# Kernel tuning notes

Hardware: AMD Instinct MI355X
Metric: run time of the kernel (lower is better)

Reference implementation:

```python
import jax, jax.numpy as jnp
import numpy as np

EPS = 1e-5
THRESHOLD = 0.2987


def conv3x3(x, w, stride=1):
    # x: [N,C,H,W], w: [O,I,3,3]
    return jax.lax.conv_general_dilated(
        x, w, window_strides=(stride, stride), padding=((1, 1), (1, 1)),
        dimension_numbers=("NCHW", "OIHW", "NCHW"))


def batchnorm_train(x, gamma, beta):
    # training-mode BN: batch statistics over (N,H,W), biased variance
    mean = jnp.mean(x, axis=(0, 2, 3), keepdims=True)
    var = jnp.var(x, axis=(0, 2, 3), keepdims=True)
    xhat = (x - mean) * jax.lax.rsqrt(var + EPS)
    return xhat * gamma[None, :, None, None] + beta[None, :, None, None]


def setup_inputs() -> dict:
    key = jax.random.key(0)
    k = jax.random.split(key, 7)
    N, C, H, W = 64, 128, 64, 64
    x = jax.random.normal(k[0], (N, C, H, W), dtype=jnp.float32)
    w1 = jax.random.normal(k[1], (C, C, 3, 3), dtype=jnp.float32) * (1.0 / np.sqrt(C * 9))
    gamma1 = jnp.ones((C,), dtype=jnp.float32)
    beta1 = jnp.zeros((C,), dtype=jnp.float32)
    w2 = jax.random.normal(k[2], (C, C, 3, 3), dtype=jnp.float32) * (1.0 / np.sqrt(C * 9))
    gamma2 = jnp.ones((C,), dtype=jnp.float32)
    beta2 = jnp.zeros((C,), dtype=jnp.float32)
    return {"x": x, "w1": w1, "gamma1": gamma1, "beta1": beta1,
            "w2": w2, "gamma2": gamma2, "beta2": beta2}


def reference(x, w1, gamma1, beta1, w2, gamma2, beta2):
    shortcut = x  # stride=1, no down_sample
    out = conv3x3(x, w1, stride=1)
    out = batchnorm_train(out, gamma1, beta1)
    out = jax.nn.relu(out)
    # per-(batch,channel) mean over H,W; zero channels whose mean < threshold
    channel_means = jnp.mean(out, axis=(2, 3))               # [N, C]
    mask = (channel_means >= THRESHOLD).astype(out.dtype)     # [N, C]
    out = out * mask[:, :, None, None]
    out = conv3x3(out, w2, stride=1)
    out = batchnorm_train(out, gamma2, beta2)
    out = out + shortcut
    out = jax.nn.relu(out)
    return out
```

## Files before the change

### kernel.cpp

```cpp
#include <hip/hip_runtime.h>

typedef short short8 __attribute__((ext_vector_type(8)));
typedef short short4v __attribute__((ext_vector_type(4)));
typedef float f32x4 __attribute__((ext_vector_type(4)));
typedef unsigned int u32;

#define EPSF 1e-5f
#define THRF 0.2987f

constexpr int N_ = 64, C_ = 128;
constexpr int PLANE = 4096;
constexpr size_t TENSOR = (size_t)N_ * C_ * PLANE;
constexpr int NHW = N_ * PLANE;
constexpr int PUNITS = 66 * 66 * 8;

__device__ __forceinline__ unsigned short f2bf(float f) {
    unsigned u = __float_as_uint(f);
    u += 0x7fffu + ((u >> 16) & 1u);
    return (unsigned short)(u >> 16);
}
__device__ __forceinline__ float bf2f(unsigned short h) {
    return __uint_as_float((unsigned)h << 16);
}
__device__ __forceinline__ void gld16(const unsigned short* g, unsigned short* l) {
    __builtin_amdgcn_global_load_lds(
        (const __attribute__((address_space(1))) u32*)g,
        (__attribute__((address_space(3))) u32*)l, 16, 0, 0);
}

__global__ __launch_bounds__(256) void prep_w_k(const float* __restrict__ w1,
                                                const float* __restrict__ w2,
                                                unsigned short* __restrict__ Wt1,
                                                unsigned short* __restrict__ Wt2) {
    int idx = blockIdx.x * 256 + threadIdx.x;
    const int sel = idx >= 147456;
    const float* src = sel ? w2 : w1;
    unsigned short* dst = sel ? Wt2 : Wt1;
    const int r = idx - sel * 147456;
    const int tap = r >> 14;
    const int rem = r & 16383;
    const int co = rem >> 7, ci = rem & 127;
    const int half = ci >> 6, csh = (ci >> 5) & 1;
    const int s = half * 18 + tap * 2 + csh;
    dst[(size_t)s * 4096 + co * 32 + (ci & 31)] = f2bf(src[(co * 128 + ci) * 9 + tap]);
}

__global__ __launch_bounds__(256) void zero_border_k(unsigned short* __restrict__ io) {
    int idx = blockIdx.x * 256 + threadIdx.x;
    if (idx >= 266240) return;
    const int plane = idx / 2080;
    const int t = idx - plane * 2080;
    int sp;
    if (t < 528) sp = t >> 3;
    else if (t < 1056) sp = 65 * 66 + ((t - 528) >> 3);
    else if (t < 1568) sp = (((t - 1056) >> 3) + 1) * 66;
    else sp = (((t - 1568) >> 3) + 1) * 66 + 65;
    const size_t off = ((size_t)plane * PUNITS + sp * 8 + (t & 7)) * 8;
    *(short8*)&io[off] = (short8){0, 0, 0, 0, 0, 0, 0, 0};
}

__global__ __launch_bounds__(256) void to_nhwc_k(const float* __restrict__ src,
                                                 unsigned short* __restrict__ dst) {
    __shared__ __align__(16) unsigned short tl[64 * 40];
    const int b = blockIdx.x;
    const int c0 = (b & 3) * 32;
    const int h  = (b >> 2) & 63;
    const int n  = b >> 8;
    const int t  = threadIdx.x;
    for (int i = t; i < 512; i += 256) {
        const int cl = i >> 4;
        const int c  = c0 + cl;
        const int w4 = (i & 15) * 4;
        float4 v = *(const float4*)&src[(size_t)(n * 128 + c) * 4096 + h * 64 + w4];
        tl[(w4 + 0) * 40 + cl] = f2bf(v.x);
        tl[(w4 + 1) * 40 + cl] = f2bf(v.y);
        tl[(w4 + 2) * 40 + cl] = f2bf(v.z);
        tl[(w4 + 3) * 40 + cl] = f2bf(v.w);
    }
    __syncthreads();
    const int w = t >> 2, cs = t & 3;
    short8 v = *(const short8*)&tl[w * 40 + cs * 8];
    const int c = c0 + cs * 8;
    const int half = c >> 6, cig = (c >> 3) & 7;
    const int colp = w + 1, rowp = h + 1;
    const size_t off = ((size_t)(half * 64 + n) * PUNITS
                        + (size_t)(rowp * 66 + colp) * 8 + (cig ^ (colp & 7))) * 8;
    *(short8*)&dst[off] = v;
}

template <int STAGE>
__global__ __launch_bounds__(256, 3) void conv_mfma_k(
    const unsigned short* __restrict__ inT, const unsigned short* __restrict__ Wt,
    const float* __restrict__ msA, const float* __restrict__ mhA,
    unsigned short* __restrict__ outB, float* __restrict__ part) {
    __shared__ __align__(16) unsigned short sIn[2112 * 8];
    __shared__ float fS[256], fQ[256];

    const int b  = (blockIdx.x & 7) * 256 + (blockIdx.x >> 3);
    const int h0 = (b & 31) * 2;
    const int n  = b >> 5;
    const int tid  = threadIdx.x;
    const int lane = tid & 63;
    const int wid  = tid >> 6;
    const int co_base = (wid >> 1) * 64;
    const int px_base = (wid & 1) * 64;
    const int lr = lane & 15;
    const int lg = lane >> 4;

    f32x4 acc[4][4];
#pragma unroll
    for (int i = 0; i < 4; ++i)
#pragma unroll
        for (int j = 0; j < 4; ++j) acc[i][j] = (f32x4){0.f, 0.f, 0.f, 0.f};

    const int nc = n * 128;
    const unsigned short* wlane = Wt + (size_t)(co_base + lr) * 32 + lg * 8;

    int ldsQ[4][2][3];
#pragma unroll
    for (int j = 0; j < 4; ++j) {
        const int px = px_base + j * 16 + lr;
        const int r = px >> 6, c = px & 63;
#pragma unroll
        for (int csh = 0; csh < 2; ++csh)
#pragma unroll
            for (int dc = 0; dc < 3; ++dc) {
                const int cig = csh * 4 + lg;
                ldsQ[j][csh][dc] = (r * 66 + c + dc) * 128 + (cig ^ ((c + dc) & 7)) * 16;
            }
    }

    auto stage_in = [&](int half) {
        const unsigned short* src =
            inT + ((size_t)(half * 64 + n) * PUNITS + (size_t)h0 * 66 * 8) * 8;
        if (STAGE == 1) {
            for (int c = wid; c < 33; c += 4)
                gld16(src + (c * 64 + lane) * 8, &sIn[c * 512]);
        } else {
            const int ncb = nc + half * 64;
            for (int i = tid; i < 2112; i += 256) {
                const int sp = i >> 3, ul = i & 7;
                const int rq = sp / 66;
                const int colp = sp - rq * 66;
                const int rp = h0 + rq;
                short8 v = {0, 0, 0, 0, 0, 0, 0, 0};
                if (rp != 0 && rp != 65 && colp != 0 && colp != 65) {
                    v = *(const short8*)&src[i * 8];
                    const int cig = ul ^ (colp & 7);
                    const int cb = ncb + cig * 8;
                    const float4 m0 = *(const float4*)&msA[cb];
                    const float4 m1 = *(const float4*)&msA[cb + 4];
                    const float4 a0 = *(const float4*)&mhA[cb];
                    const float4 a1 = *(const float4*)&mhA[cb + 4];
                    short8 w;
                    w[0] = (short)f2bf(fmaxf(fmaf(bf2f((unsigned short)v[0]), m0.x, a0.x), 0.f));
                    w[1] = (short)f2bf(fmaxf(fmaf(bf2f((unsigned short)v[1]), m0.y, a0.y), 0.f));
                    w[2] = (short)f2bf(fmaxf(fmaf(bf2f((unsigned short)v[2]), m0.z, a0.z), 0.f));
                    w[3] = (short)f2bf(fmaxf(fmaf(bf2f((unsigned short)v[3]), m0.w, a0.w), 0.f));
                    w[4] = (short)f2bf(fmaxf(fmaf(bf2f((unsigned short)v[4]), m1.x, a1.x), 0.f));
                    w[5] = (short)f2bf(fmaxf(fmaf(bf2f((unsigned short)v[5]), m1.y, a1.y), 0.f));
                    w[6] = (short)f2bf(fmaxf(fmaf(bf2f((unsigned short)v[6]), m1.z, a1.z), 0.f));
                    w[7] = (short)f2bf(fmaxf(fmaf(bf2f((unsigned short)v[7]), m1.w, a1.w), 0.f));
                    v = w;
                }
                *(short8*)&sIn[i * 8] = v;
            }
        }
    };

    auto ldw2 = [&](short8* dst, const unsigned short* p) {
#pragma unroll
        for (int i = 0; i < 4; ++i)
            dst[i] = *(const short8*)&p[i * 512];
    };
    auto ldb = [&](short8* bfv, int dr, int dc, int csh) {
#pragma unroll
        for (int j = 0; j < 4; ++j)
            bfv[j] = *(const short8*)((const char*)sIn + ldsQ[j][csh][dc] + dr * 8448);
    };
    auto mm = [&](short8* af, short8* bfv) {
        __builtin_amdgcn_s_setprio(1);
#pragma unroll
        for (int i = 0; i < 4; ++i)
#pragma unroll
            for (int j = 0; j < 4; ++j)
                acc[i][j] = __builtin_amdgcn_mfma_f32_16x16x32_bf16(af[i], bfv[j],
                                                                    acc[i][j], 0, 0, 0);
        __builtin_amdgcn_s_setprio(0);
    };

    short8 afA[4], afB[4], bfv[4];
    const unsigned short* wpA = wlane;
    const unsigned short* wpB = wlane + 4096;

    stage_in(0);
    ldw2(afA, wpA);
    ldw2(afB, wpB);
    __syncthreads();

#pragma unroll
    for (int half = 0; half < 2; ++half) {
#pragma unroll
        for (int it = 0; it < 9; ++it) {
            const int dr = it / 3, dc = it - dr * 3;
            ldb(bfv, dr, dc, 0);
            mm(afA, bfv);
            if (it < 8) { wpA += 8192; ldw2(afA, wpA); }
            ldb(bfv, dr, dc, 1);
            mm(afB, bfv);
            if (it < 8) { wpB += 8192; ldw2(afB, wpB); }
        }
        if (half == 0) {
            wpA += 8192; ldw2(afA, wpA);
            wpB += 8192; ldw2(afB, wpB);
            __syncthreads();
            stage_in(1);
            __syncthreads();
        }
    }

#pragma unroll
    for (int i = 0; i < 4; ++i)
#pragma unroll
        for (int q = 0; q < 4; ++q) {
            float v = acc[i][0][q] + acc[i][1][q] + acc[i][2][q] + acc[i][3][q];
            float w = acc[i][0][q] * acc[i][0][q] + acc[i][1][q] * acc[i][1][q]
                    + acc[i][2][q] * acc[i][2][q] + acc[i][3][q] * acc[i][3][q];
#pragma unroll
            for (int m = 1; m < 16; m <<= 1) {
                v += __shfl_xor(v, m);
                w += __shfl_xor(w, m);
            }
            if (lr == 0) {
                const int colocal = i * 16 + lg * 4 + q;
                fS[wid * 64 + colocal] = v;
                fQ[wid * 64 + colocal] = w;
            }
        }
    __syncthreads();
    if (tid < 128) {
        const int grp = tid >> 6, cl = tid & 63;
        part[(size_t)b * 256 + tid]       = fS[(grp * 2) * 64 + cl] + fS[(grp * 2 + 1) * 64 + cl];
        part[(size_t)b * 256 + 128 + tid] = fQ[(grp * 2) * 64 + cl] + fQ[(grp * 2 + 1) * 64 + cl];
    }

    if (STAGE == 1) {
        const int h = h0 + (px_base >> 6);
        const int rowp = h + 1;
        const size_t plane = (size_t)((co_base >> 6) * 64 + n) * PUNITS * 8;
        const int pg = lg >> 1;
#pragma unroll
        for (int j = 0; j < 4; ++j) {
            const int w = j * 16 + lr;
            const int colp = w + 1;
            const size_t spoff = plane + (size_t)(rowp * 66 + colp) * 8 * 8;
#pragma unroll
            for (int i = 0; i < 4; ++i) {
                u32 p0 = ((u32)f2bf(acc[i][j][1]) << 16) | f2bf(acc[i][j][0]);
                u32 p1 = ((u32)f2bf(acc[i][j][3]) << 16) | f2bf(acc[i][j][2]);
                const u32 q0 = __shfl_xor(p0, 16);
                const u32 q1 = __shfl_xor(p1, 16);
                if ((lg & 1) == 0) {
                    const int cig = (i * 2 + pg) & 7;
                    u32 st4[4] = {p0, p1, q0, q1};
                    *(short8*)&outB[spoff + (size_t)(cig ^ (colp & 7)) * 8] =
                        *(const short8*)st4;
                }
            }
        }
    } else {
        const size_t outN = (size_t)n * 128 * 4096;
#pragma unroll
        for (int i = 0; i < 4; ++i) {
            const int cob = co_base + i * 16 + lg * 4;
#pragma unroll
            for (int q = 0; q < 4; ++q) {
                unsigned short* op = outB + outN + (size_t)(cob + q) * 4096
                                     + h0 * 64 + px_base + lr;
#pragma unroll
                for (int j = 0; j < 4; ++j) op[j * 16] = f2bf(acc[i][j][q]);
            }
        }
    }
}

__global__ __launch_bounds__(256) void bn_finalize_k(const float* __restrict__ part,
                                                     const float* __restrict__ gamma,
                                                     const float* __restrict__ beta,
                                                     float* __restrict__ st) {
    const int c = blockIdx.x;
    float s = 0.f, q = 0.f;
    for (int b = threadIdx.x; b < 2048; b += 256) {
        s += part[(size_t)b * 256 + c];
        q += part[(size_t)b * 256 + 128 + c];
    }
    __shared__ float rs[256], rq[256];
    rs[threadIdx.x] = s; rq[threadIdx.x] = q;
    __syncthreads();
    for (int o = 128; o > 0; o >>= 1) {
        if (threadIdx.x < o) {
            rs[threadIdx.x] += rs[threadIdx.x + o];
            rq[threadIdx.x] += rq[threadIdx.x + o];
        }
        __syncthreads();
    }
    if (threadIdx.x == 0) {
        const float inv  = 1.f / (float)NHW;
        const float mean = rs[0] * inv;
        const float var  = rq[0] * inv - mean * mean;
        const float sc   = gamma[c] * rsqrtf(var + EPSF);
        st[c]       = sc;
        st[C_ + c]  = fmaf(-mean, sc, beta[c]);
    }
}

__global__ __launch_bounds__(256) void maskpart_k(const unsigned short* __restrict__ y1,
                                                  const float* __restrict__ st,
                                                  float* __restrict__ qsum) {
    const int blk = blockIdx.x;
    const int n = blk >> 3, half = (blk >> 2) & 1, rq = blk & 3;
    const int t = threadIdx.x;
    const int colg = t & 63;
    const int p = t >> 6;
    const int colp = 1 + colg;
    float scv[2][8], shv[2][8], a[2][8];
#pragma unroll
    for (int k = 0; k < 2; ++k)
#pragma unroll
        for (int e = 0; e < 8; ++e) {
            const int c = half * 64 + (2 * p + k) * 8 + e;
            scv[k][e] = st[c];
            shv[k][e] = st[128 + c];
            a[k][e] = 0.f;
        }
    const size_t plane = (size_t)(half * 64 + n) * PUNITS * 8;
    for (int rowp = rq * 16 + 1; rowp <= rq * 16 + 16; ++rowp) {
        const int sp = rowp * 66 + colp;
#pragma unroll
        for (int k = 0; k < 2; ++k) {
            const int cig = 2 * p + k;
            short8 v = *(const short8*)&y1[plane + ((size_t)sp * 8 + (cig ^ (colp & 7))) * 8];
#pragma unroll
            for (int e = 0; e < 8; ++e)
                a[k][e] += fmaxf(fmaf(bf2f((unsigned short)v[e]), scv[k][e], shv[k][e]), 0.f);
        }
    }
    __shared__ float lds[256][16];
#pragma unroll
    for (int k = 0; k < 2; ++k)
#pragma unroll
        for (int e = 0; e < 8; ++e) lds[t][k * 8 + e] = a[k][e];
    __syncthreads();
    if (t < 64) {
        const int cig = t >> 3, e = t & 7, p2 = cig >> 1, k2 = cig & 1;
        float s = 0.f;
        for (int cg = 0; cg < 64; ++cg) s += lds[p2 * 64 + cg][k2 * 8 + e];
        qsum[(size_t)blk * 64 + t] = s;
    }
}

__global__ void maskfin_k(const float* __restrict__ qsum, const float* __restrict__ st,
                          float* __restrict__ msA, float* __restrict__ mhA) {
    const int n = blockIdx.x, c = threadIdx.x;
    if (c >= 128) return;
    const int half = c >> 6, cl = c & 63;
    float s = 0.f;
#pragma unroll
    for (int rq = 0; rq < 4; ++rq)
        s += qsum[(size_t)(n * 8 + half * 4 + rq) * 64 + cl];
    const float m = (s * (1.f / 4096.f) >= THRF) ? 1.f : 0.f;
    msA[n * 128 + c] = st[c] * m;
    mhA[n * 128 + c] = st[128 + c] * m;
}

__global__ __launch_bounds__(256) void final_k(const unsigned short* __restrict__ y3,
                                               const float* __restrict__ x,
                                               const float* __restrict__ st,
                                               float* __restrict__ out) {
    const size_t total8 = TENSOR / 8;
    for (size_t g = (size_t)blockIdx.x * 256 + threadIdx.x; g < total8;
         g += (size_t)gridDim.x * 256) {
        const int c = (int)((g >> 9) & (C_ - 1));
        const float sc = st[c], sh = st[C_ + c];
        short8 yv = *(const short8*)&y3[g * 8];
        float4 a0 = ((const float4*)x)[g * 2];
        float4 a1 = ((const float4*)x)[g * 2 + 1];
        float4 o0, o1;
        o0.x = fmaxf(fmaf(bf2f((unsigned short)yv[0]), sc, sh) + a0.x, 0.f);
        o0.y = fmaxf(fmaf(bf2f((unsigned short)yv[1]), sc, sh) + a0.y, 0.f);
        o0.z = fmaxf(fmaf(bf2f((unsigned short)yv[2]), sc, sh) + a0.z, 0.f);
        o0.w = fmaxf(fmaf(bf2f((unsigned short)yv[3]), sc, sh) + a0.w, 0.f);
        o1.x = fmaxf(fmaf(bf2f((unsigned short)yv[4]), sc, sh) + a1.x, 0.f);
        o1.y = fmaxf(fmaf(bf2f((unsigned short)yv[5]), sc, sh) + a1.y, 0.f);
        o1.z = fmaxf(fmaf(bf2f((unsigned short)yv[6]), sc, sh) + a1.z, 0.f);
        o1.w = fmaxf(fmaf(bf2f((unsigned short)yv[7]), sc, sh) + a1.w, 0.f);
        ((float4*)out)[g * 2]     = o0;
        ((float4*)out)[g * 2 + 1] = o1;
    }
}

extern "C" void kernel_launch(void* const* d_in, const int* in_sizes, int n_in,
                              void* d_out, int out_size, void* d_ws, size_t ws_size,
                              hipStream_t stream) {
    const float* x  = (const float*)d_in[0];
    const float* w1 = (const float*)d_in[1];
    const float* g1 = (const float*)d_in[2];
    const float* b1 = (const float*)d_in[3];
    const float* w2 = (const float*)d_in[4];
    const float* g2 = (const float*)d_in[5];
    const float* b2 = (const float*)d_in[6];
    float* out = (float*)d_out;

    unsigned short* y1 = (unsigned short*)d_out;

    char* wsb = (char*)d_ws;
    unsigned short* io  = (unsigned short*)wsb;
    unsigned short* y3b = (unsigned short*)wsb;
    unsigned short* Wt1 = (unsigned short*)(wsb + (size_t)71368704);
    unsigned short* Wt2 = Wt1 + 147456;
    float* part = (float*)(wsb + (size_t)71368704 + 589824);
    float* st1  = part + 2048 * 256;
    float* st2  = st1 + 256;
    float* msA  = st2 + 256;
    float* mhA  = msA + 64 * 128;
    float* qsum = mhA + 64 * 128;

    prep_w_k<<<1152, 256, 0, stream>>>(w1, w2, Wt1, Wt2);
    zero_border_k<<<1040, 256, 0, stream>>>(io);
    to_nhwc_k<<<16384, 256, 0, stream>>>(x, io);
    conv_mfma_k<1><<<2048, 256, 0, stream>>>(io, Wt1, nullptr, nullptr, y1, part);
    bn_finalize_k<<<128, 256, 0, stream>>>(part, g1, b1, st1);
    maskpart_k<<<512, 256, 0, stream>>>(y1, st1, qsum);
    maskfin_k<<<64, 128, 0, stream>>>(qsum, st1, msA, mhA);
    conv_mfma_k<2><<<2048, 256, 0, stream>>>(y1, Wt2, msA, mhA, y3b, part);
    bn_finalize_k<<<128, 256, 0, stream>>>(part, g2, b2, st2);
    final_k<<<8192, 256, 0, stream>>>(y3b, x, st2, out);
}
```

Before: 310.6 us.

## Double-buffer conv weight fragments and fold border zeroing into layout kernel

The conv kernel now keeps two sets of A/B weight fragment registers and prefetches weights two steps ahead instead of one. This gives global weight loads more time to land before the MFMAs that need them. Separately, the border-zeroing kernel is merged into the NHWC conversion kernel as extra blocks, which saves one launch. Holding twice the weight registers raises VGPR pressure and could lower occupancy.

Result: slower. 326.9 us (+5.3%).

```diff
diff --git a/kernel.cpp b/kernel.cpp
--- a/kernel.cpp
+++ b/kernel.cpp
@@ -45,24 +45,25 @@
     dst[(size_t)s * 4096 + co * 32 + (ci & 31)] = f2bf(src[(co * 128 + ci) * 9 + tap]);
 }
 
-__global__ __launch_bounds__(256) void zero_border_k(unsigned short* __restrict__ io) {
-    int idx = blockIdx.x * 256 + threadIdx.x;
-    if (idx >= 266240) return;
-    const int plane = idx / 2080;
-    const int t = idx - plane * 2080;
-    int sp;
-    if (t < 528) sp = t >> 3;
-    else if (t < 1056) sp = 65 * 66 + ((t - 528) >> 3);
-    else if (t < 1568) sp = (((t - 1056) >> 3) + 1) * 66;
-    else sp = (((t - 1568) >> 3) + 1) * 66 + 65;
-    const size_t off = ((size_t)plane * PUNITS + sp * 8 + (t & 7)) * 8;
-    *(short8*)&io[off] = (short8){0, 0, 0, 0, 0, 0, 0, 0};
-}
-
 __global__ __launch_bounds__(256) void to_nhwc_k(const float* __restrict__ src,
                                                  unsigned short* __restrict__ dst) {
+    const int b = blockIdx.x;
+    if (b >= 16384) {
+        int idx = (b - 16384) * 256 + threadIdx.x;
+        if (idx < 266240) {
+            const int plane = idx / 2080;
+            const int t = idx - plane * 2080;
+            int sp;
+            if (t < 528) sp = t >> 3;
+            else if (t < 1056) sp = 65 * 66 + ((t - 528) >> 3);
+            else if (t < 1568) sp = (((t - 1056) >> 3) + 1) * 66;
+            else sp = (((t - 1568) >> 3) + 1) * 66 + 65;
+            const size_t off = ((size_t)plane * PUNITS + sp * 8 + (t & 7)) * 8;
+            *(short8*)&dst[off] = (short8){0, 0, 0, 0, 0, 0, 0, 0};
+        }
+        return;
+    }
     __shared__ __align__(16) unsigned short tl[64 * 40];
-    const int b = blockIdx.x;
     const int c0 = (b & 3) * 32;
     const int h  = (b >> 2) & 63;
     const int n  = b >> 8;
@@ -189,33 +190,38 @@
         __builtin_amdgcn_s_setprio(0);
     };
 
-    short8 afA[4], afB[4], bfv[4];
-    const unsigned short* wpA = wlane;
-    const unsigned short* wpB = wlane + 4096;
+    short8 afA0[4], afB0[4], afA1[4], afB1[4], bfv[4];
 
     stage_in(0);
-    ldw2(afA, wpA);
-    ldw2(afB, wpB);
+    ldw2(afA0, wlane);
+    ldw2(afB0, wlane + (size_t)1 * 4096);
+    ldw2(afA1, wlane + (size_t)2 * 4096);
+    ldw2(afB1, wlane + (size_t)3 * 4096);
     __syncthreads();
 
 #pragma unroll
-    for (int half = 0; half < 2; ++half) {
-#pragma unroll
-        for (int it = 0; it < 9; ++it) {
-            const int dr = it / 3, dc = it - dr * 3;
-            ldb(bfv, dr, dc, 0);
-            mm(afA, bfv);
-            if (it < 8) { wpA += 8192; ldw2(afA, wpA); }
-            ldb(bfv, dr, dc, 1);
-            mm(afB, bfv);
-            if (it < 8) { wpB += 8192; ldw2(afB, wpB); }
-        }
-        if (half == 0) {
-            wpA += 8192; ldw2(afA, wpA);
-            wpB += 8192; ldw2(afB, wpB);
+    for (int it = 0; it < 18; ++it) {
+        const int tap = it % 9;
+        const int dr = tap / 3, dc = tap - dr * 3;
+        if (it == 9) {
             __syncthreads();
             stage_in(1);
             __syncthreads();
+        }
+        if ((it & 1) == 0) {
+            ldb(bfv, dr, dc, 0);
+            mm(afA0, bfv);
+            if (2 * it + 4 < 36) ldw2(afA0, wlane + (size_t)(2 * it + 4) * 4096);
+            ldb(bfv, dr, dc, 1);
+            mm(afB0, bfv);
+            if (2 * it + 5 < 36) ldw2(afB0, wlane + (size_t)(2 * it + 5) * 4096);
+        } else {
+            ldb(bfv, dr, dc, 0);
+            mm(afA1, bfv);
+            if (2 * it + 4 < 36) ldw2(afA1, wlane + (size_t)(2 * it + 4) * 4096);
+            ldb(bfv, dr, dc, 1);
+            mm(afB1, bfv);
+            if (2 * it + 5 < 36) ldw2(afB1, wlane + (size_t)(2 * it + 5) * 4096);
         }
     }
 
@@ -426,8 +432,7 @@
     float* qsum = mhA + 64 * 128;
 
     prep_w_k<<<1152, 256, 0, stream>>>(w1, w2, Wt1, Wt2);
-    zero_border_k<<<1040, 256, 0, stream>>>(io);
-    to_nhwc_k<<<16384, 256, 0, stream>>>(x, io);
+    to_nhwc_k<<<17424, 256, 0, stream>>>(x, io);
     conv_mfma_k<1><<<2048, 256, 0, stream>>>(io, Wt1, nullptr, nullptr, y1, part);
     bn_finalize_k<<<128, 256, 0, stream>>>(part, g1, b1, st1);
     maskpart_k<<<512, 256, 0, stream>>>(y1, st1, qsum);
```
